# Kernel optimization log

Measured on AMD Instinct MI355X. Metric: run time of the kernel, lower is better.

Reference implementation:

```python
import jax, jax.numpy as jnp
import numpy as np

B, H, W = 16, 128, 128
NUM_SAMPLES, HID = 16, 256


def setup_inputs() -> dict:
    key = jax.random.key(0)
    ks = jax.random.split(key, 12)
    inp = {
        "x": jax.random.uniform(ks[0], (B, H, W, 2), jnp.float32) * 2.0 - 1.0,
        "sample_idx": jax.random.randint(ks[1], (B,), 0, NUM_SAMPLES),
        "shift_vectors": jax.random.normal(ks[2], (NUM_SAMPLES, 2), jnp.float32) * 0.05,
        "rotation_angle": jax.random.normal(ks[3], (NUM_SAMPLES, 1), jnp.float32) * 0.05,
        "color_scales": 1.0 + jax.random.normal(ks[4], (NUM_SAMPLES, 3), jnp.float32) * 0.05,
        "color_shifts": jax.random.normal(ks[5], (NUM_SAMPLES, 3), jnp.float32) * 0.05,
        "W1": jax.random.normal(ks[6], (2, HID), jnp.float32) / np.sqrt(2.0),
        "b1": jnp.zeros((HID,), jnp.float32),
        "W2": jax.random.normal(ks[7], (HID, HID), jnp.float32) / np.sqrt(HID),
        "b2": jnp.zeros((HID,), jnp.float32),
        "W3": jax.random.normal(ks[8], (HID, HID), jnp.float32) / np.sqrt(HID),
        "b3": jnp.zeros((HID,), jnp.float32),
        "W4": jax.random.normal(ks[9], (HID, 3), jnp.float32) / np.sqrt(HID),
        "b4": jnp.zeros((3,), jnp.float32),
    }
    return inp


def reference(x, sample_idx, shift_vectors, rotation_angle, color_scales, color_shifts,
              W1, b1, W2, b2, W3, b3, W4, b4):
    # Per-sample affine coordinate transform (vectorized gather + batched 2x3 affine).
    shift = shift_vectors[sample_idx]            # [B,2] -> (dy, dx)
    dy, dx = shift[:, 0], shift[:, 1]
    ang = rotation_angle[sample_idx, 0]          # [B]
    c, s = jnp.cos(ang), jnp.sin(ang)
    rot = jnp.stack([jnp.stack([c, -s], -1),
                     jnp.stack([s, c], -1)], -2)  # [B,2,2]
    trans = jnp.stack([dx, dy], -1)               # [B,2]
    coords = jnp.einsum('bij,bhwj->bhwi', rot, x) + trans[:, None, None, :]

    # INR decoder MLP: coords -> RGB
    h = jax.nn.relu(coords @ W1 + b1)
    h = jax.nn.relu(h @ W2 + b2)
    h = jax.nn.relu(h @ W3 + b3)
    out = h @ W4 + b4                             # [B,H,W,3]

    # Per-sample color affine, skipped for reference sample idx==0.
    scales = color_scales[sample_idx][:, None, None, :]
    shifts = color_shifts[sample_idx][:, None, None, :]
    mask = (sample_idx != 0)[:, None, None, None]
    out = jnp.where(mask, out * scales + shifts, out)
    return out, dx, dy
```

## Files before the change

kernel.cpp:

```cpp
#include <hip/hip_runtime.h>
#include <math.h>

typedef _Float16 half8  __attribute__((ext_vector_type(8)));
typedef _Float16 half4v __attribute__((ext_vector_type(4)));
typedef _Float16 half2v __attribute__((ext_vector_type(2)));
typedef float    f32x4  __attribute__((ext_vector_type(4)));

#define W1OFF 0
#define W2OFF 8192
#define W3OFF 73728
#define W4OFF 139264
#define SWTOT 143360
#define OUT_PIX (16*128*128)

__global__ void inr_prep(const float* __restrict__ W1, const float* __restrict__ W2,
                         const float* __restrict__ W3, const float* __restrict__ W4,
                         const int* __restrict__ sidx, const float* __restrict__ sv,
                         _Float16* __restrict__ wsw, float* __restrict__ outtail)
{
    int tid = blockIdx.x * 256 + threadIdx.x;
    if (tid < 16) {
        int si = sidx[tid];
        outtail[tid]      = sv[2*si + 1];
        outtail[16 + tid] = sv[2*si + 0];
    }
    if (tid >= SWTOT) return;
    int kind, rel;
    if      (tid < W2OFF) { kind = 0; rel = tid; }
    else if (tid < W3OFF) { kind = 1; rel = tid - W2OFF; }
    else if (tid < W4OFF) { kind = 2; rel = tid - W3OFF; }
    else                  { kind = 3; rel = tid - W4OFF; }
    int j    = rel & 7;
    int lane = (rel >> 3) & 63;
    int blk  = rel >> 9;
    int q = lane >> 4, ln = lane & 15;
    float val;
    if (kind == 3) {
        int m = ln;
        int k = blk * 32 + q * 8 + j;
        val = (m < 3) ? W4[k*3 + m] : 0.0f;
    } else {
        int MT = blk & 15, kkb = blk >> 4;
        int m = MT*16 + ln;
        int k = kkb*32 + q*8 + j;
        if      (kind == 0) val = (k < 2) ? W1[k*256 + m] : 0.0f;
        else if (kind == 1) val = W2[k*256 + m];
        else                val = W3[k*256 + m];
    }
    wsw[tid] = (_Float16)val;
}

template<int NKK>
__device__ __forceinline__ void do_layer(const half8* __restrict__ Asw,
                                         const float* __restrict__ bias,
                                         _Float16* hbuf, int w, int q, int ln, int lane)
{
    f32x4 acc[4][8];
#pragma unroll
    for (int mt = 0; mt < 4; ++mt)
#pragma unroll
        for (int nt = 0; nt < 8; ++nt)
            acc[mt][nt] = (f32x4){0.f, 0.f, 0.f, 0.f};

#pragma unroll
    for (int kkb = 0; kkb < NKK; ++kkb) {
        half8 aw[4];
#pragma unroll
        for (int mt = 0; mt < 4; ++mt)
            aw[mt] = Asw[(kkb*16 + 4*w + mt)*64 + lane];
        half8 bf[8];
        int g = kkb*4 + q;
#pragma unroll
        for (int nt = 0; nt < 8; ++nt)
            bf[nt] = *(const half8*)&hbuf[g*1024 + (16*nt + ln)*8];
#pragma unroll
        for (int nt = 0; nt < 8; ++nt)
#pragma unroll
            for (int mt = 0; mt < 4; ++mt)
                acc[mt][nt] = __builtin_amdgcn_mfma_f32_16x16x32_f16(aw[mt], bf[nt], acc[mt][nt], 0, 0, 0);
    }
    __syncthreads();
#pragma unroll
    for (int mt = 0; mt < 4; ++mt) {
        int hid0 = 64*w + 16*mt + 4*q;
        f32x4 bv = *(const f32x4*)&bias[hid0];
        int g = hid0 >> 3;
        int o = hid0 & 7;
#pragma unroll
        for (int nt = 0; nt < 8; ++nt) {
            int pixel = 16*nt + ln;
            f32x4 a = acc[mt][nt];
            half4v hv;
            hv[0] = (_Float16)fmaxf(a[0] + bv[0], 0.f);
            hv[1] = (_Float16)fmaxf(a[1] + bv[1], 0.f);
            hv[2] = (_Float16)fmaxf(a[2] + bv[2], 0.f);
            hv[3] = (_Float16)fmaxf(a[3] + bv[3], 0.f);
            *(half4v*)&hbuf[g*1024 + pixel*8 + o] = hv;
        }
    }
    __syncthreads();
}

__launch_bounds__(256, 2)
__global__ void inr_fused(const float* __restrict__ x, const int* __restrict__ sidx_p,
                          const float* __restrict__ sv, const float* __restrict__ ra,
                          const float* __restrict__ cs, const float* __restrict__ csh,
                          const float* __restrict__ b1, const float* __restrict__ b2,
                          const float* __restrict__ b3, const float* __restrict__ b4,
                          const _Float16* __restrict__ wsw, float* __restrict__ out)
{
    __shared__ __align__(16) _Float16 hbuf[32768];
    int t = threadIdx.x;
    int lane = t & 63, w = t >> 6, q = lane >> 4, ln = lane & 15;
    int pixbase = blockIdx.x * 128;
    int b = pixbase >> 14;
    int sidx = sidx_p[b];
    float dy = sv[2*sidx], dx = sv[2*sidx + 1];
    float ang = ra[sidx];
    float sn, cn;
    sincosf(ang, &sn, &cn);

    if (t < 128) {
        int p = t;
        float x0 = x[(pixbase + p)*2 + 0];
        float x1 = x[(pixbase + p)*2 + 1];
        float u = cn*x0 - sn*x1 + dx;
        float v = sn*x0 + cn*x1 + dy;
        half8 z;
#pragma unroll
        for (int i = 0; i < 8; ++i) z[i] = (_Float16)0.0f;
#pragma unroll
        for (int g = 1; g < 4; ++g)
            *(half8*)&hbuf[g*1024 + p*8] = z;
        z[0] = (_Float16)u; z[1] = (_Float16)v;
        *(half8*)&hbuf[0*1024 + p*8] = z;
    }
    __syncthreads();

    const half8* wsw8 = (const half8*)wsw;
    do_layer<1>(wsw8,                b1, hbuf, w, q, ln, lane);
    do_layer<8>(wsw8 + (W2OFF >> 3), b2, hbuf, w, q, ln, lane);
    do_layer<8>(wsw8 + (W3OFF >> 3), b3, hbuf, w, q, ln, lane);

    const half8* w4p = wsw8 + (W4OFF >> 3);
    f32x4 a4[2];
    a4[0] = (f32x4){0.f,0.f,0.f,0.f};
    a4[1] = (f32x4){0.f,0.f,0.f,0.f};
#pragma unroll
    for (int kkb = 0; kkb < 8; ++kkb) {
        half8 aw = w4p[kkb*64 + lane];
#pragma unroll
        for (int i = 0; i < 2; ++i) {
            int pixel = 16*(2*w + i) + ln;
            half8 bf = *(const half8*)&hbuf[(kkb*4 + q)*1024 + pixel*8];
            a4[i] = __builtin_amdgcn_mfma_f32_16x16x32_f16(aw, bf, a4[i], 0, 0, 0);
        }
    }
    if (q == 0) {
        bool doc = (sidx != 0);
        float s0 = cs[sidx*3+0], s1 = cs[sidx*3+1], s2 = cs[sidx*3+2];
        float t0 = csh[sidx*3+0], t1 = csh[sidx*3+1], t2 = csh[sidx*3+2];
        float bb0 = b4[0], bb1 = b4[1], bb2 = b4[2];
#pragma unroll
        for (int i = 0; i < 2; ++i) {
            int gp = pixbase + 16*(2*w + i) + ln;
            float v0 = a4[i][0] + bb0;
            float v1 = a4[i][1] + bb1;
            float v2 = a4[i][2] + bb2;
            if (doc) { v0 = v0*s0 + t0; v1 = v1*s1 + t1; v2 = v2*s2 + t2; }
            out[gp*3 + 0] = v0;
            out[gp*3 + 1] = v1;
            out[gp*3 + 2] = v2;
        }
    }
}

extern "C" void kernel_launch(void* const* d_in, const int* in_sizes, int n_in,
                              void* d_out, int out_size, void* d_ws, size_t ws_size,
                              hipStream_t stream)
{
    const float* x    = (const float*)d_in[0];
    const int*   sidx = (const int*)  d_in[1];
    const float* sv   = (const float*)d_in[2];
    const float* ra   = (const float*)d_in[3];
    const float* cs   = (const float*)d_in[4];
    const float* csh  = (const float*)d_in[5];
    const float* W1   = (const float*)d_in[6];
    const float* b1   = (const float*)d_in[7];
    const float* W2   = (const float*)d_in[8];
    const float* b2   = (const float*)d_in[9];
    const float* W3   = (const float*)d_in[10];
    const float* b3   = (const float*)d_in[11];
    const float* W4   = (const float*)d_in[12];
    const float* b4   = (const float*)d_in[13];
    float* out = (float*)d_out;
    _Float16* wsw = (_Float16*)d_ws;

    inr_prep<<<SWTOT/256, 256, 0, stream>>>(W1, W2, W3, W4, sidx, sv, wsw, out + OUT_PIX*3);
    inr_fused<<<OUT_PIX/128, 256, 0, stream>>>(x, sidx, sv, ra, cs, csh,
                                               b1, b2, b3, b4, wsw, out);
}
```

Baseline: 144.7 us.

## Split block work across 8 waves with 2D wave tiling over hidden and pixels

Doubles the block to 512 threads and arranges the 8 waves as a 4x2 grid, so each wave computes a 64-hidden by 64-pixel tile instead of 64x128. This halves the accumulator registers per wave and raises the requested occupancy via launch bounds, which should help hide latency. The last layer now uses one MFMA per wave instead of two. In exchange each wave loads the same weight fragments as before over half as many pixels, so weight traffic per MFMA doubles, and the larger block synchronises more waves at each barrier.

```diff
diff --git a/kernel.cpp b/kernel.cpp
--- a/kernel.cpp
+++ b/kernel.cpp
@@ -3,7 +3,6 @@
 
 typedef _Float16 half8  __attribute__((ext_vector_type(8)));
 typedef _Float16 half4v __attribute__((ext_vector_type(4)));
-typedef _Float16 half2v __attribute__((ext_vector_type(2)));
 typedef float    f32x4  __attribute__((ext_vector_type(4)));
 
 #define W1OFF 0
@@ -53,13 +52,14 @@
 template<int NKK>
 __device__ __forceinline__ void do_layer(const half8* __restrict__ Asw,
                                          const float* __restrict__ bias,
-                                         _Float16* hbuf, int w, int q, int ln, int lane)
+                                         _Float16* hbuf, int wm, int wn,
+                                         int q, int ln, int lane)
 {
-    f32x4 acc[4][8];
+    f32x4 acc[4][4];
 #pragma unroll
     for (int mt = 0; mt < 4; ++mt)
 #pragma unroll
-        for (int nt = 0; nt < 8; ++nt)
+        for (int nt = 0; nt < 4; ++nt)
             acc[mt][nt] = (f32x4){0.f, 0.f, 0.f, 0.f};
 
 #pragma unroll
@@ -67,14 +67,14 @@
         half8 aw[4];
 #pragma unroll
         for (int mt = 0; mt < 4; ++mt)
-            aw[mt] = Asw[(kkb*16 + 4*w + mt)*64 + lane];
-        half8 bf[8];
+            aw[mt] = Asw[(kkb*16 + 4*wm + mt)*64 + lane];
+        half8 bf[4];
         int g = kkb*4 + q;
 #pragma unroll
-        for (int nt = 0; nt < 8; ++nt)
-            bf[nt] = *(const half8*)&hbuf[g*1024 + (16*nt + ln)*8];
+        for (int nt = 0; nt < 4; ++nt)
+            bf[nt] = *(const half8*)&hbuf[g*1024 + (wn*64 + 16*nt + ln)*8];
 #pragma unroll
-        for (int nt = 0; nt < 8; ++nt)
+        for (int nt = 0; nt < 4; ++nt)
 #pragma unroll
             for (int mt = 0; mt < 4; ++mt)
                 acc[mt][nt] = __builtin_amdgcn_mfma_f32_16x16x32_f16(aw[mt], bf[nt], acc[mt][nt], 0, 0, 0);
@@ -82,13 +82,13 @@
     __syncthreads();
 #pragma unroll
     for (int mt = 0; mt < 4; ++mt) {
-        int hid0 = 64*w + 16*mt + 4*q;
+        int hid0 = 64*wm + 16*mt + 4*q;
         f32x4 bv = *(const f32x4*)&bias[hid0];
         int g = hid0 >> 3;
         int o = hid0 & 7;
 #pragma unroll
-        for (int nt = 0; nt < 8; ++nt) {
-            int pixel = 16*nt + ln;
+        for (int nt = 0; nt < 4; ++nt) {
+            int pixel = wn*64 + 16*nt + ln;
             f32x4 a = acc[mt][nt];
             half4v hv;
             hv[0] = (_Float16)fmaxf(a[0] + bv[0], 0.f);
@@ -101,7 +101,7 @@
     __syncthreads();
 }
 
-__launch_bounds__(256, 2)
+__launch_bounds__(512, 4)
 __global__ void inr_fused(const float* __restrict__ x, const int* __restrict__ sidx_p,
                           const float* __restrict__ sv, const float* __restrict__ ra,
                           const float* __restrict__ cs, const float* __restrict__ csh,
@@ -112,6 +112,7 @@
     __shared__ __align__(16) _Float16 hbuf[32768];
     int t = threadIdx.x;
     int lane = t & 63, w = t >> 6, q = lane >> 4, ln = lane & 15;
+    int wm = w & 3, wn = w >> 2;
     int pixbase = blockIdx.x * 128;
     int b = pixbase >> 14;
     int sidx = sidx_p[b];
@@ -138,40 +139,30 @@
     __syncthreads();
 
     const half8* wsw8 = (const half8*)wsw;
-    do_layer<1>(wsw8,                b1, hbuf, w, q, ln, lane);
-    do_layer<8>(wsw8 + (W2OFF >> 3), b2, hbuf, w, q, ln, lane);
-    do_layer<8>(wsw8 + (W3OFF >> 3), b3, hbuf, w, q, ln, lane);
+    do_layer<1>(wsw8,                b1, hbuf, wm, wn, q, ln, lane);
+    do_layer<8>(wsw8 + (W2OFF >> 3), b2, hbuf, wm, wn, q, ln, lane);
+    do_layer<8>(wsw8 + (W3OFF >> 3), b3, hbuf, wm, wn, q, ln, lane);
 
     const half8* w4p = wsw8 + (W4OFF >> 3);
-    f32x4 a4[2];
-    a4[0] = (f32x4){0.f,0.f,0.f,0.f};
-    a4[1] = (f32x4){0.f,0.f,0.f,0.f};
+    f32x4 a4 = (f32x4){0.f,0.f,0.f,0.f};
 #pragma unroll
     for (int kkb = 0; kkb < 8; ++kkb) {
         half8 aw = w4p[kkb*64 + lane];
-#pragma unroll
-        for (int i = 0; i < 2; ++i) {
-            int pixel = 16*(2*w + i) + ln;
-            half8 bf = *(const half8*)&hbuf[(kkb*4 + q)*1024 + pixel*8];
-            a4[i] = __builtin_amdgcn_mfma_f32_16x16x32_f16(aw, bf, a4[i], 0, 0, 0);
-        }
+        half8 bf = *(const half8*)&hbuf[(kkb*4 + q)*1024 + (16*w + ln)*8];
+        a4 = __builtin_amdgcn_mfma_f32_16x16x32_f16(aw, bf, a4, 0, 0, 0);
     }
     if (q == 0) {
         bool doc = (sidx != 0);
         float s0 = cs[sidx*3+0], s1 = cs[sidx*3+1], s2 = cs[sidx*3+2];
         float t0 = csh[sidx*3+0], t1 = csh[sidx*3+1], t2 = csh[sidx*3+2];
-        float bb0 = b4[0], bb1 = b4[1], bb2 = b4[2];
-#pragma unroll
-        for (int i = 0; i < 2; ++i) {
-            int gp = pixbase + 16*(2*w + i) + ln;
-            float v0 = a4[i][0] + bb0;
-            float v1 = a4[i][1] + bb1;
-            float v2 = a4[i][2] + bb2;
-            if (doc) { v0 = v0*s0 + t0; v1 = v1*s1 + t1; v2 = v2*s2 + t2; }
-            out[gp*3 + 0] = v0;
-            out[gp*3 + 1] = v1;
-            out[gp*3 + 2] = v2;
-        }
+        float v0 = a4[0] + b4[0];
+        float v1 = a4[1] + b4[1];
+        float v2 = a4[2] + b4[2];
+        if (doc) { v0 = v0*s0 + t0; v1 = v1*s1 + t1; v2 = v2*s2 + t2; }
+        int gp = pixbase + 16*w + ln;
+        out[gp*3 + 0] = v0;
+        out[gp*3 + 1] = v1;
+        out[gp*3 + 2] = v2;
     }
 }
 
@@ -197,6 +188,6 @@
     _Float16* wsw = (_Float16*)d_ws;
 
     inr_prep<<<SWTOT/256, 256, 0, stream>>>(W1, W2, W3, W4, sidx, sv, wsw, out + OUT_PIX*3);
-    inr_fused<<<OUT_PIX/128, 256, 0, stream>>>(x, sidx, sv, ra, cs, csh,
+    inr_fused<<<OUT_PIX/128, 512, 0, stream>>>(x, sidx, sv, ra, cs, csh,
                                                b1, b2, b3, b4, wsw, out);
 }
```

Measured after the change: 150.0 us. 3.7% more time.

## Retile layer GEMMs as 2x2 warp grid and use packed fp16 conversion

Applied to the files above, without the earlier changes.

Each wave now computes 128 hidden units by 64 pixels (8 M-tiles × 4 N-tiles) instead of 64 hidden by all 128 pixels. Per k-step this loads 8 weight fragments from global/L2 and 4 activation fragments from LDS, rather than 4 and 8. That cuts LDS read traffic but doubles weight-fragment loads per wave. The epilogue also switches to packed round-toward-zero fp16 conversion (cvt_pkrtz), which slightly changes rounding.

```diff
diff --git a/kernel.cpp b/kernel.cpp
--- a/kernel.cpp
+++ b/kernel.cpp
@@ -3,7 +3,7 @@
 
 typedef _Float16 half8  __attribute__((ext_vector_type(8)));
 typedef _Float16 half4v __attribute__((ext_vector_type(4)));
-typedef _Float16 half2v __attribute__((ext_vector_type(2)));
+typedef __fp16   fp16x2 __attribute__((ext_vector_type(2)));
 typedef float    f32x4  __attribute__((ext_vector_type(4)));
 
 #define W1OFF 0
@@ -53,48 +53,51 @@
 template<int NKK>
 __device__ __forceinline__ void do_layer(const half8* __restrict__ Asw,
                                          const float* __restrict__ bias,
-                                         _Float16* hbuf, int w, int q, int ln, int lane)
-{
-    f32x4 acc[4][8];
-#pragma unroll
-    for (int mt = 0; mt < 4; ++mt)
-#pragma unroll
-        for (int nt = 0; nt < 8; ++nt)
+                                         _Float16* hbuf, int wm, int wn,
+                                         int q, int ln, int lane)
+{
+    f32x4 acc[8][4];
+#pragma unroll
+    for (int mt = 0; mt < 8; ++mt)
+#pragma unroll
+        for (int nt = 0; nt < 4; ++nt)
             acc[mt][nt] = (f32x4){0.f, 0.f, 0.f, 0.f};
 
 #pragma unroll
     for (int kkb = 0; kkb < NKK; ++kkb) {
-        half8 aw[4];
-#pragma unroll
-        for (int mt = 0; mt < 4; ++mt)
-            aw[mt] = Asw[(kkb*16 + 4*w + mt)*64 + lane];
-        half8 bf[8];
+        half8 aw[8];
+#pragma unroll
+        for (int mt = 0; mt < 8; ++mt)
+            aw[mt] = Asw[(kkb*16 + wm*8 + mt)*64 + lane];
+        half8 bf[4];
         int g = kkb*4 + q;
 #pragma unroll
-        for (int nt = 0; nt < 8; ++nt)
-            bf[nt] = *(const half8*)&hbuf[g*1024 + (16*nt + ln)*8];
-#pragma unroll
-        for (int nt = 0; nt < 8; ++nt)
-#pragma unroll
-            for (int mt = 0; mt < 4; ++mt)
+        for (int nt = 0; nt < 4; ++nt)
+            bf[nt] = *(const half8*)&hbuf[g*1024 + (wn*64 + 16*nt + ln)*8];
+#pragma unroll
+        for (int nt = 0; nt < 4; ++nt)
+#pragma unroll
+            for (int mt = 0; mt < 8; ++mt)
                 acc[mt][nt] = __builtin_amdgcn_mfma_f32_16x16x32_f16(aw[mt], bf[nt], acc[mt][nt], 0, 0, 0);
     }
     __syncthreads();
 #pragma unroll
-    for (int mt = 0; mt < 4; ++mt) {
-        int hid0 = 64*w + 16*mt + 4*q;
+    for (int mt = 0; mt < 8; ++mt) {
+        int hid0 = wm*128 + 16*mt + 4*q;
         f32x4 bv = *(const f32x4*)&bias[hid0];
         int g = hid0 >> 3;
         int o = hid0 & 7;
 #pragma unroll
-        for (int nt = 0; nt < 8; ++nt) {
-            int pixel = 16*nt + ln;
+        for (int nt = 0; nt < 4; ++nt) {
+            int pixel = wn*64 + 16*nt + ln;
             f32x4 a = acc[mt][nt];
+            fp16x2 lo = __builtin_amdgcn_cvt_pkrtz(fmaxf(a[0] + bv[0], 0.f),
+                                                   fmaxf(a[1] + bv[1], 0.f));
+            fp16x2 hi = __builtin_amdgcn_cvt_pkrtz(fmaxf(a[2] + bv[2], 0.f),
+                                                   fmaxf(a[3] + bv[3], 0.f));
             half4v hv;
-            hv[0] = (_Float16)fmaxf(a[0] + bv[0], 0.f);
-            hv[1] = (_Float16)fmaxf(a[1] + bv[1], 0.f);
-            hv[2] = (_Float16)fmaxf(a[2] + bv[2], 0.f);
-            hv[3] = (_Float16)fmaxf(a[3] + bv[3], 0.f);
+            hv[0] = (_Float16)lo[0]; hv[1] = (_Float16)lo[1];
+            hv[2] = (_Float16)hi[0]; hv[3] = (_Float16)hi[1];
             *(half4v*)&hbuf[g*1024 + pixel*8 + o] = hv;
         }
     }
@@ -112,6 +115,7 @@
     __shared__ __align__(16) _Float16 hbuf[32768];
     int t = threadIdx.x;
     int lane = t & 63, w = t >> 6, q = lane >> 4, ln = lane & 15;
+    int wm = w & 1, wn = w >> 1;
     int pixbase = blockIdx.x * 128;
     int b = pixbase >> 14;
     int sidx = sidx_p[b];
@@ -138,9 +142,9 @@
     __syncthreads();
 
     const half8* wsw8 = (const half8*)wsw;
-    do_layer<1>(wsw8,                b1, hbuf, w, q, ln, lane);
-    do_layer<8>(wsw8 + (W2OFF >> 3), b2, hbuf, w, q, ln, lane);
-    do_layer<8>(wsw8 + (W3OFF >> 3), b3, hbuf, w, q, ln, lane);
+    do_layer<1>(wsw8,                b1, hbuf, wm, wn, q, ln, lane);
+    do_layer<8>(wsw8 + (W2OFF >> 3), b2, hbuf, wm, wn, q, ln, lane);
+    do_layer<8>(wsw8 + (W3OFF >> 3), b3, hbuf, wm, wn, q, ln, lane);
 
     const half8* w4p = wsw8 + (W4OFF >> 3);
     f32x4 a4[2];
```

Measured after the change: 148.6 us. +2.7%, slower.
